# Kernel tuning notes

Hardware: AMD Instinct MI355X
Metric: run time of the kernel (lower is better)

Reference implementation:

```python
import jax, jax.numpy as jnp
import numpy as np

N = 100000   # num_nodes
E = 1600000  # num_edges
IN, HID, OUT = 128, 128, 64  # in_ft, 2*out_ft, out_ft


def setup_inputs() -> dict:
    key = jax.random.key(0)
    ks = jax.random.split(key, 8)
    x = jax.random.normal(ks[0], (N, IN), dtype=jnp.float32)
    edge_index = jax.random.randint(ks[1], (2, E), 0, N, dtype=jnp.int32)
    # Glorot-style init for GCNConv linear weights
    W1 = jax.random.normal(ks[2], (IN, HID), dtype=jnp.float32) / np.sqrt(IN).astype(np.float32)
    b1 = jnp.zeros((HID,), dtype=jnp.float32)
    W2 = jax.random.normal(ks[3], (HID, OUT), dtype=jnp.float32) / np.sqrt(HID).astype(np.float32)
    b2 = jnp.zeros((OUT,), dtype=jnp.float32)
    a = jnp.array([0.25], dtype=jnp.float32)  # shared PReLU slope (nn.PReLU default)
    return {"x": x, "edge_index": edge_index, "W1": W1, "b1": b1, "W2": W2, "b2": b2, "a": a}


def reference(x, edge_index, W1, b1, W2, b2, a):
    # PyG GCNConv semantics: add self-loops, symmetric normalization
    # norm_e = deg(src)^-1/2 * deg(dst)^-1/2, out[dst] += norm_e * (x @ W)[src] + bias
    src, dst = edge_index[0], edge_index[1]
    loops = jnp.arange(N, dtype=src.dtype)
    s = jnp.concatenate([src, loops])  # [E+N]
    d = jnp.concatenate([dst, loops])  # [E+N]
    deg = jax.ops.segment_sum(jnp.ones_like(d, dtype=x.dtype), d, num_segments=N)
    dis = jax.lax.rsqrt(deg)  # deg >= 1 thanks to self-loops
    norm = (dis[s] * dis[d])[:, None]  # [E+N, 1]

    def gcn_conv(h, W, b):
        hw = h @ W                                   # dense transform [N, F_out]
        msgs = hw[s] * norm                          # gather + scale  [E+N, F_out]
        return jax.ops.segment_sum(msgs, d, num_segments=N) + b  # scatter-add

    prelu = lambda v: jnp.where(v >= 0, v, a * v)

    h = prelu(gcn_conv(x, W1, b1))   # dropout p=0.0 -> identity
    return prelu(gcn_conv(h, W2, b2))
```

## Files before the change

kernel.cpp:

```cpp
#include <hip/hip_runtime.h>

#define N_NODES 100000
#define N_EDGES 1600000
#define BSH 9
#define NB  196
#define EPB 4096
#define CAPSH 14

typedef short bf16x8 __attribute__((ext_vector_type(8)));
typedef float f32x4 __attribute__((ext_vector_type(4)));
typedef float f32x2 __attribute__((ext_vector_type(2)));


__device__ __forceinline__ unsigned pack_bf16x2(float a, float b) {
    unsigned ua = __float_as_uint(a), ub = __float_as_uint(b);
    unsigned ra = (ua + 0x7fffu + ((ua >> 16) & 1u)) >> 16;
    unsigned rb = (ub + 0x7fffu + ((ub >> 16) & 1u)) >> 16;
    return ra | (rb << 16);
}
__device__ __forceinline__ unsigned short bf16_rne(float f) {
    unsigned u = __float_as_uint(f);
    return (unsigned short)((u + 0x7fffu + ((u >> 16) & 1u)) >> 16);
}
__device__ __forceinline__ float bf_lo(unsigned v) { return __uint_as_float(v << 16); }
__device__ __forceinline__ float bf_hi(unsigned v) { return __uint_as_float(v & 0xffff0000u); }
__device__ __forceinline__ f32x2 unpk(unsigned u) {
    f32x2 r;
    r.x = __uint_as_float(u << 16);
    r.y = __uint_as_float(u & 0xffff0000u);
    return r;
}


__global__ void cursor_init_k(int* __restrict__ cursor) {
    int b = threadIdx.x;
    if (b < NB) cursor[b] = b << CAPSH;
}

__global__ __launch_bounds__(256) void bin_k(const int* __restrict__ src,
                                             const int* __restrict__ dst,
                                             int* __restrict__ cursor,
                                             unsigned* __restrict__ binned, int E) {
    __shared__ int lhist[256];
    __shared__ int lcur[256];
    int tid = threadIdx.x;
    lhist[tid] = 0;
    __syncthreads();
    int e0 = blockIdx.x * EPB;
#pragma unroll
    for (int i = 0; i < EPB / 256; ++i) {
        int e = e0 + i * 256 + tid;
        if (e < E) atomicAdd(&lhist[dst[e] >> BSH], 1);
    }
    __syncthreads();
    {
        int c = lhist[tid];
        lcur[tid] = (tid < NB && c > 0) ? atomicAdd(&cursor[tid], c) : 0;
    }
    __syncthreads();
#pragma unroll
    for (int i = 0; i < EPB / 256; ++i) {
        int e = e0 + i * 256 + tid;
        if (e < E) {
            int d = dst[e];
            int b = d >> BSH;
            int pos = atomicAdd(&lcur[b], 1);
            if (pos < ((b + 1) << CAPSH))
                binned[pos] = ((unsigned)(d & ((1 << BSH) - 1)) << 17) | (unsigned)src[e];
        }
    }
}

__global__ void bucket_scan_k(const int* __restrict__ cursor, int* __restrict__ bucket_base) {
    __shared__ int s[256];
    int tid = threadIdx.x;
    int v = (tid < NB) ? (cursor[tid] - (tid << CAPSH)) : 0;
    s[tid] = v; __syncthreads();
    for (int off = 1; off < 256; off <<= 1) {
        int t = 0;
        if (tid >= off) t = s[tid - off];
        __syncthreads();
        s[tid] += t;
        __syncthreads();
    }
    if (tid < NB) bucket_base[tid] = s[tid] - v;
}

__global__ __launch_bounds__(256) void deg_dis_k(const unsigned* __restrict__ binned,
                                                 const int* __restrict__ cursor,
                                                 const int* __restrict__ bucket_base,
                                                 int* __restrict__ row_start,
                                                 float* __restrict__ dis, int n, int E) {
    __shared__ int lcnt[1 << BSH];
    __shared__ int ls[256];
    int b = blockIdx.x, tid = threadIdx.x;
    for (int j = tid; j < (1 << BSH); j += 256) lcnt[j] = 0;
    __syncthreads();
    int base = b << CAPSH;
    int total = cursor[b] - base;
    for (int i = tid; i < total; i += 256)
        atomicAdd(&lcnt[binned[base + i] >> 17], 1);
    __syncthreads();
    int v0 = lcnt[2 * tid], v1 = lcnt[2 * tid + 1];
    int sv = v0 + v1;
    ls[tid] = sv;
    __syncthreads();
    for (int off = 1; off < 256; off <<= 1) {
        int t = 0;
        if (tid >= off) t = ls[tid - off];
        __syncthreads();
        ls[tid] += t;
        __syncthreads();
    }
    int pre = ls[tid] - sv;
    int nbase = b << BSH;
    int bb = bucket_base[b];
    int node0 = nbase + 2 * tid, node1 = node0 + 1;
    if (node0 < n) {
        row_start[node0] = bb + pre;
        dis[node0] = rsqrtf((float)(v0 + 1));
    }
    if (node1 < n) {
        row_start[node1] = bb + pre + v0;
        dis[node1] = rsqrtf((float)(v1 + 1));
    }
    if (b == NB - 1 && tid == 255) row_start[n] = E;
}

__global__ __launch_bounds__(256) void csr_k(const unsigned* __restrict__ binned,
                                             const int* __restrict__ cursor,
                                             const int* __restrict__ row_start,
                                             const float* __restrict__ dis,
                                             uint2* __restrict__ edge, int n) {
    __shared__ int lfill[1 << BSH];
    int b = blockIdx.x, tid = threadIdx.x;
    int nbase = b << BSH;
    for (int j = tid; j < (1 << BSH); j += 256) {
        int node = nbase + j;
        lfill[j] = (node < n) ? row_start[node] : 0;
    }
    __syncthreads();
    int base = b << CAPSH;
    int total = cursor[b] - base;
    for (int i = base + tid; i < base + total; i += 256) {
        unsigned u = binned[i];
        int s = u & 0x1FFFFu;
        int dl = u >> 17;
        int pos = atomicAdd(&lfill[dl], 1);
        edge[pos] = make_uint2((unsigned)s, __float_as_uint(dis[s] * dis[nbase + dl]));
    }
}


__global__ void wt_k(const float* __restrict__ W, unsigned short* __restrict__ Wt, int C) {
    int t = blockIdx.x * 256 + threadIdx.x;
    if (t >= 128 * C) return;
    int k = t / C, c = t % C;
    int g = k >> 3, j = k & 7;
    Wt[c * 128 + ((g ^ (c & 7)) << 3) + j] = bf16_rne(W[t]);
}


template <int OUTF, bool INBF>
__global__ __launch_bounds__(256) void gemm_mfma_k(const void* __restrict__ Xv,
                                                   const unsigned short* __restrict__ Wt,
                                                   unsigned short* __restrict__ Y, int nrows) {
    constexpr int CT = OUTF / 16;
    __shared__ short lds_w[OUTF * 128];
    int tid = threadIdx.x;
    {
        const uint4* srcp = (const uint4*)Wt;
        uint4* dstp = (uint4*)lds_w;
        for (int i = tid; i < OUTF * 16; i += 256) dstp[i] = srcp[i];
    }
    __syncthreads();
    int lane = tid & 63;
    int r16 = lane & 15, kq = lane >> 4;
    int rbase = blockIdx.x * 128 + (tid >> 6) * 32;
    f32x4 acc[2][CT] = {};
#pragma unroll
    for (int kk = 0; kk < 4; ++kk) {
        int k0 = kk * 32 + kq * 8;
        bf16x8 a[2];
#pragma unroll
        for (int rt = 0; rt < 2; ++rt) {
            int row = rbase + rt * 16 + r16;
            if (row < nrows) {
                if constexpr (INBF) {
                    a[rt] = *(const bf16x8*)((const unsigned short*)Xv + (size_t)row * 128 + k0);
                } else {
                    const float* xp = (const float*)Xv + (size_t)row * 128 + k0;
                    float4 f0 = *(const float4*)xp;
                    float4 f1 = *(const float4*)(xp + 4);
                    uint4 uu = make_uint4(pack_bf16x2(f0.x, f0.y), pack_bf16x2(f0.z, f0.w),
                                          pack_bf16x2(f1.x, f1.y), pack_bf16x2(f1.z, f1.w));
                    a[rt] = *(bf16x8*)&uu;
                }
            } else {
                bf16x8 z = {0, 0, 0, 0, 0, 0, 0, 0};
                a[rt] = z;
            }
        }
#pragma unroll
        for (int c = 0; c < CT; ++c) {
            int col = c * 16 + r16;
            int gp = (kk * 4 + kq) ^ (col & 7);
            bf16x8 b = *(const bf16x8*)&lds_w[col * 128 + gp * 8];
            acc[0][c] = __builtin_amdgcn_mfma_f32_16x16x32_bf16(a[0], b, acc[0][c], 0, 0, 0);
            acc[1][c] = __builtin_amdgcn_mfma_f32_16x16x32_bf16(a[1], b, acc[1][c], 0, 0, 0);
        }
    }
#pragma unroll
    for (int rt = 0; rt < 2; ++rt) {
#pragma unroll
        for (int c = 0; c < CT; ++c) {
#pragma unroll
            for (int r = 0; r < 4; ++r) {
                int row = rbase + rt * 16 + kq * 4 + r;
                if (row < nrows)
                    Y[(size_t)row * OUTF + c * 16 + r16] = bf16_rne(acc[rt][c][r]);
            }
        }
    }
}


__global__ void agg1_k(const unsigned* __restrict__ hw, const int* __restrict__ row_start,
                       const uint2* __restrict__ edge, const float* __restrict__ dis,
                       const float* __restrict__ bias, const float* __restrict__ aslope,
                       unsigned* __restrict__ out, int n) {
    int wid = (blockIdx.x * 256 + threadIdx.x) >> 6;
    int lane = threadIdx.x & 63;
    if (wid >= n) return;
    int g = lane >> 4;
    unsigned li = lane & 15;
    unsigned rowoff = li << 4;
    const char* hwb = (const char*)hw;
    const char* edb = (const char*)edge;
    f32x2 acc[4] = {};
    int e0 = row_start[wid], e1 = row_start[wid + 1];
    for (int e = e0; e < e1; e += 16) {
        uint2 ed[4];
        uint4 v[4];
#pragma unroll
        for (int u = 0; u < 4; ++u) {
            int ee = e + u * 4 + g;
            unsigned ec = (unsigned)((ee < e1) ? ee : (e1 - 1));
            ed[u] = *(const uint2*)(edb + (ec << 3));
        }
#pragma unroll
        for (int u = 0; u < 4; ++u)
            v[u] = *(const uint4*)(hwb + ((ed[u].x << 8) | rowoff));
#pragma unroll
        for (int u = 0; u < 4; ++u) {
            float nr = (e + u * 4 + g < e1) ? __uint_as_float(ed[u].y) : 0.f;
            f32x2 nr2 = {nr, nr};
            acc[0] += unpk(v[u].x) * nr2;
            acc[1] += unpk(v[u].y) * nr2;
            acc[2] += unpk(v[u].z) * nr2;
            acc[3] += unpk(v[u].w) * nr2;
        }
    }
#pragma unroll
    for (int j = 0; j < 4; ++j) {
        acc[j].x += __shfl_xor(acc[j].x, 16, 64);
        acc[j].y += __shfl_xor(acc[j].y, 16, 64);
        acc[j].x += __shfl_xor(acc[j].x, 32, 64);
        acc[j].y += __shfl_xor(acc[j].y, 32, 64);
    }
    if (g == 0) {
        float dn = dis[wid];
        f32x2 sw2 = {dn * dn, dn * dn};
        uint4 v = *(const uint4*)(hwb + (((unsigned)wid << 8) | rowoff));
        acc[0] += unpk(v.x) * sw2;
        acc[1] += unpk(v.y) * sw2;
        acc[2] += unpk(v.z) * sw2;
        acc[3] += unpk(v.w) * sw2;
        float4 b0 = ((const float4*)bias)[li * 2];
        float4 b1 = ((const float4*)bias)[li * 2 + 1];
        float al = aslope[0];
        float r[8] = {acc[0].x + b0.x, acc[0].y + b0.y, acc[1].x + b0.z, acc[1].y + b0.w,
                      acc[2].x + b1.x, acc[2].y + b1.y, acc[3].x + b1.z, acc[3].y + b1.w};
#pragma unroll
        for (int j = 0; j < 8; ++j) r[j] = (r[j] >= 0.f) ? r[j] : al * r[j];
        uint4 o = make_uint4(pack_bf16x2(r[0], r[1]), pack_bf16x2(r[2], r[3]),
                             pack_bf16x2(r[4], r[5]), pack_bf16x2(r[6], r[7]));
        *(uint4*)(out + (size_t)wid * 64 + li * 4) = o;
    }
}

__global__ void agg2_k(const unsigned* __restrict__ hw, const int* __restrict__ row_start,
                       const uint2* __restrict__ edge, const float* __restrict__ dis,
                       const float* __restrict__ bias, const float* __restrict__ aslope,
                       float* __restrict__ out, int n) {
    int wid = (blockIdx.x * 256 + threadIdx.x) >> 6;
    int lane = threadIdx.x & 63;
    if (wid >= n) return;
    int g = lane >> 4;
    unsigned li = lane & 15;
    unsigned rowoff = li << 3;
    const char* hwb = (const char*)hw;
    const char* edb = (const char*)edge;
    f32x2 acc[2] = {};
    int e0 = row_start[wid], e1 = row_start[wid + 1];
    for (int e = e0; e < e1; e += 16) {
        uint2 ed[4];
        uint2 v[4];
#pragma unroll
        for (int u = 0; u < 4; ++u) {
            int ee = e + u * 4 + g;
            unsigned ec = (unsigned)((ee < e1) ? ee : (e1 - 1));
            ed[u] = *(const uint2*)(edb + (ec << 3));
        }
#pragma unroll
        for (int u = 0; u < 4; ++u)
            v[u] = *(const uint2*)(hwb + ((ed[u].x << 7) | rowoff));
#pragma unroll
        for (int u = 0; u < 4; ++u) {
            float nr = (e + u * 4 + g < e1) ? __uint_as_float(ed[u].y) : 0.f;
            f32x2 nr2 = {nr, nr};
            acc[0] += unpk(v[u].x) * nr2;
            acc[1] += unpk(v[u].y) * nr2;
        }
    }
#pragma unroll
    for (int j = 0; j < 2; ++j) {
        acc[j].x += __shfl_xor(acc[j].x, 16, 64);
        acc[j].y += __shfl_xor(acc[j].y, 16, 64);
        acc[j].x += __shfl_xor(acc[j].x, 32, 64);
        acc[j].y += __shfl_xor(acc[j].y, 32, 64);
    }
    if (g == 0) {
        float dn = dis[wid];
        f32x2 sw2 = {dn * dn, dn * dn};
        uint2 v = *(const uint2*)(hwb + (((unsigned)wid << 7) | rowoff));
        acc[0] += unpk(v.x) * sw2;
        acc[1] += unpk(v.y) * sw2;
        float4 b = ((const float4*)bias)[li];
        float al = aslope[0];
        float r[4] = {acc[0].x + b.x, acc[0].y + b.y, acc[1].x + b.z, acc[1].y + b.w};
#pragma unroll
        for (int j = 0; j < 4; ++j) r[j] = (r[j] >= 0.f) ? r[j] : al * r[j];
        *(float4*)(out + (size_t)wid * 64 + li * 4) = make_float4(r[0], r[1], r[2], r[3]);
    }
}


extern "C" void kernel_launch(void* const* d_in, const int* in_sizes, int n_in,
                              void* d_out, int out_size, void* d_ws, size_t ws_size,
                              hipStream_t stream) {
    const float* x  = (const float*)d_in[0];
    const int*   ei = (const int*)d_in[1];
    const int*   src = ei;
    const int*   dst = ei + N_EDGES;
    const float* W1 = (const float*)d_in[2];
    const float* b1 = (const float*)d_in[3];
    const float* W2 = (const float*)d_in[4];
    const float* b2 = (const float*)d_in[5];
    const float* a  = (const float*)d_in[6];
    float* out = (float*)d_out;

    char* ws = (char*)d_ws;
    size_t off = 0;
    auto alloc = [&](size_t bytes) -> void* {
        void* p = ws + off;
        off += (bytes + 255) & ~(size_t)255;
        return p;
    };
    int*            row_start = (int*)alloc((size_t)(N_NODES + 1) * 4);
    float*          dis       = (float*)alloc((size_t)N_NODES * 4);
    int*            cursor    = (int*)alloc(NB * 4);
    int*            bbase     = (int*)alloc(NB * 4);
    unsigned*       binned    = (unsigned*)alloc((size_t)NB * (1 << CAPSH) * 4);
    uint2*          edge      = (uint2*)alloc((size_t)N_EDGES * 8);
    unsigned*       hw1       = (unsigned*)alloc((size_t)N_NODES * 64 * 4);
    unsigned*       hbuf      = (unsigned*)alloc((size_t)N_NODES * 64 * 4);
    unsigned*       hw2       = (unsigned*)alloc((size_t)N_NODES * 32 * 4);
    unsigned short* Wt1       = (unsigned short*)alloc(128 * 128 * 2);
    unsigned short* Wt2       = (unsigned short*)alloc(64 * 128 * 2);

    int gB = (N_EDGES + EPB - 1) / EPB;

    wt_k<<<64, 256, 0, stream>>>(W1, Wt1, 128);
    wt_k<<<32, 256, 0, stream>>>(W2, Wt2, 64);

    cursor_init_k<<<1, 256, 0, stream>>>(cursor);
    bin_k<<<gB, 256, 0, stream>>>(src, dst, cursor, binned, N_EDGES);
    bucket_scan_k<<<1, 256, 0, stream>>>(cursor, bbase);
    deg_dis_k<<<NB, 256, 0, stream>>>(binned, cursor, bbase, row_start, dis, N_NODES, N_EDGES);
    csr_k<<<NB, 256, 0, stream>>>(binned, cursor, row_start, dis, edge, N_NODES);

    int gG = (N_NODES + 127) / 128;
    int gA = (N_NODES + 3) / 4;

    gemm_mfma_k<128, false><<<gG, 256, 0, stream>>>(x, Wt1, (unsigned short*)hw1, N_NODES);
    agg1_k<<<gA, 256, 0, stream>>>(hw1, row_start, edge, dis, b1, a, hbuf, N_NODES);
    gemm_mfma_k<64, true><<<gG, 256, 0, stream>>>(hbuf, Wt2, (unsigned short*)hw2, N_NODES);
    agg2_k<<<gA, 256, 0, stream>>>(hw2, row_start, edge, dis, b2, a, out, N_NODES);
}
```

Baseline: 207.6 us.

## Fuse setup kernels, co-launch binning with GEMM1, and remap aggregation to four nodes per wave

The weight-transpose and cursor-init kernels are merged into one setup launch. Edge binning and the first dense GEMM now run in a single grid, so independent memory-bound and MFMA work can overlap and one launch is removed. Both aggregation kernels now give each 16-lane group its own node instead of spreading one node across a wave, which removes the cross-group shuffle reduction. The cost is that lanes diverge across nodes with different degrees inside a wave, and the fused kernel reserves 32KB of LDS even in binning blocks, which may lower their occupancy.

```diff
diff --git a/kernel.cpp b/kernel.cpp
--- a/kernel.cpp
+++ b/kernel.cpp
@@ -6,6 +6,8 @@
 #define NB  196
 #define EPB 4096
 #define CAPSH 14
+#define GB  ((N_EDGES + EPB - 1) / EPB)
+#define GG  ((N_NODES + 127) / 128)
 
 typedef short bf16x8 __attribute__((ext_vector_type(8)));
 typedef float f32x4 __attribute__((ext_vector_type(4)));
@@ -22,8 +24,6 @@
     unsigned u = __float_as_uint(f);
     return (unsigned short)((u + 0x7fffu + ((u >> 16) & 1u)) >> 16);
 }
-__device__ __forceinline__ float bf_lo(unsigned v) { return __uint_as_float(v << 16); }
-__device__ __forceinline__ float bf_hi(unsigned v) { return __uint_as_float(v & 0xffff0000u); }
 __device__ __forceinline__ f32x2 unpk(unsigned u) {
     f32x2 r;
     r.x = __uint_as_float(u << 16);
@@ -32,41 +32,114 @@
 }
 
 
-__global__ void cursor_init_k(int* __restrict__ cursor) {
-    int b = threadIdx.x;
-    if (b < NB) cursor[b] = b << CAPSH;
-}
-
-__global__ __launch_bounds__(256) void bin_k(const int* __restrict__ src,
-                                             const int* __restrict__ dst,
-                                             int* __restrict__ cursor,
-                                             unsigned* __restrict__ binned, int E) {
+__device__ __forceinline__ void wt_body(const float* W, unsigned short* Wt, int C, int bid) {
+    int t = bid * 256 + threadIdx.x;
+    if (t >= 128 * C) return;
+    int k = t / C, c = t % C;
+    int g = k >> 3, j = k & 7;
+    Wt[c * 128 + ((g ^ (c & 7)) << 3) + j] = bf16_rne(W[t]);
+}
+
+__global__ void setup_k(const float* __restrict__ W1, unsigned short* __restrict__ Wt1,
+                        const float* __restrict__ W2, unsigned short* __restrict__ Wt2,
+                        int* __restrict__ cursor) {
+    int b = blockIdx.x;
+    if (b < 64) { wt_body(W1, Wt1, 128, b); }
+    else if (b < 96) { wt_body(W2, Wt2, 64, b - 64); }
+    else {
+        int t = threadIdx.x;
+        if (t < NB) cursor[t] = t << CAPSH;
+    }
+}
+
+
+__global__ __launch_bounds__(256) void bin_gemm1_k(
+        const int* __restrict__ src, const int* __restrict__ dst,
+        int* __restrict__ cursor, unsigned* __restrict__ binned,
+        const float* __restrict__ X, const unsigned short* __restrict__ Wt,
+        unsigned short* __restrict__ Y) {
     __shared__ int lhist[256];
     __shared__ int lcur[256];
+    __shared__ short lds_w[128 * 128];
     int tid = threadIdx.x;
-    lhist[tid] = 0;
-    __syncthreads();
-    int e0 = blockIdx.x * EPB;
-#pragma unroll
-    for (int i = 0; i < EPB / 256; ++i) {
-        int e = e0 + i * 256 + tid;
-        if (e < E) atomicAdd(&lhist[dst[e] >> BSH], 1);
-    }
-    __syncthreads();
+
+    if (blockIdx.x < GB) {
+        lhist[tid] = 0;
+        __syncthreads();
+        int e0 = blockIdx.x * EPB;
+#pragma unroll
+        for (int i = 0; i < EPB / 256; ++i) {
+            int e = e0 + i * 256 + tid;
+            if (e < N_EDGES) atomicAdd(&lhist[dst[e] >> BSH], 1);
+        }
+        __syncthreads();
+        {
+            int c = lhist[tid];
+            lcur[tid] = (tid < NB && c > 0) ? atomicAdd(&cursor[tid], c) : 0;
+        }
+        __syncthreads();
+#pragma unroll
+        for (int i = 0; i < EPB / 256; ++i) {
+            int e = e0 + i * 256 + tid;
+            if (e < N_EDGES) {
+                int d = dst[e];
+                int b = d >> BSH;
+                int pos = atomicAdd(&lcur[b], 1);
+                if (pos < ((b + 1) << CAPSH))
+                    binned[pos] = ((unsigned)(d & ((1 << BSH) - 1)) << 17) | (unsigned)src[e];
+            }
+        }
+        return;
+    }
+
     {
-        int c = lhist[tid];
-        lcur[tid] = (tid < NB && c > 0) ? atomicAdd(&cursor[tid], c) : 0;
-    }
-    __syncthreads();
-#pragma unroll
-    for (int i = 0; i < EPB / 256; ++i) {
-        int e = e0 + i * 256 + tid;
-        if (e < E) {
-            int d = dst[e];
-            int b = d >> BSH;
-            int pos = atomicAdd(&lcur[b], 1);
-            if (pos < ((b + 1) << CAPSH))
-                binned[pos] = ((unsigned)(d & ((1 << BSH) - 1)) << 17) | (unsigned)src[e];
+        const uint4* srcp = (const uint4*)Wt;
+        uint4* dstp = (uint4*)lds_w;
+        for (int i = tid; i < 128 * 16; i += 256) dstp[i] = srcp[i];
+    }
+    __syncthreads();
+    int lane = tid & 63;
+    int r16 = lane & 15, kq = lane >> 4;
+    int rbase = (blockIdx.x - GB) * 128 + (tid >> 6) * 32;
+    f32x4 acc[2][8] = {};
+#pragma unroll
+    for (int kk = 0; kk < 4; ++kk) {
+        int k0 = kk * 32 + kq * 8;
+        bf16x8 a[2];
+#pragma unroll
+        for (int rt = 0; rt < 2; ++rt) {
+            int row = rbase + rt * 16 + r16;
+            if (row < N_NODES) {
+                const float* xp = X + (size_t)row * 128 + k0;
+                float4 f0 = *(const float4*)xp;
+                float4 f1 = *(const float4*)(xp + 4);
+                uint4 uu = make_uint4(pack_bf16x2(f0.x, f0.y), pack_bf16x2(f0.z, f0.w),
+                                      pack_bf16x2(f1.x, f1.y), pack_bf16x2(f1.z, f1.w));
+                a[rt] = *(bf16x8*)&uu;
+            } else {
+                bf16x8 z = {0, 0, 0, 0, 0, 0, 0, 0};
+                a[rt] = z;
+            }
+        }
+#pragma unroll
+        for (int c = 0; c < 8; ++c) {
+            int col = c * 16 + r16;
+            int gp = (kk * 4 + kq) ^ (col & 7);
+            bf16x8 b = *(const bf16x8*)&lds_w[col * 128 + gp * 8];
+            acc[0][c] = __builtin_amdgcn_mfma_f32_16x16x32_bf16(a[0], b, acc[0][c], 0, 0, 0);
+            acc[1][c] = __builtin_amdgcn_mfma_f32_16x16x32_bf16(a[1], b, acc[1][c], 0, 0, 0);
+        }
+    }
+#pragma unroll
+    for (int rt = 0; rt < 2; ++rt) {
+#pragma unroll
+        for (int c = 0; c < 8; ++c) {
+#pragma unroll
+            for (int r = 0; r < 4; ++r) {
+                int row = rbase + rt * 16 + kq * 4 + r;
+                if (row < N_NODES)
+                    Y[(size_t)row * 128 + c * 16 + r16] = bf16_rne(acc[rt][c][r]);
+            }
         }
     }
 }
@@ -152,32 +225,21 @@
 }
 
 
-__global__ void wt_k(const float* __restrict__ W, unsigned short* __restrict__ Wt, int C) {
-    int t = blockIdx.x * 256 + threadIdx.x;
-    if (t >= 128 * C) return;
-    int k = t / C, c = t % C;
-    int g = k >> 3, j = k & 7;
-    Wt[c * 128 + ((g ^ (c & 7)) << 3) + j] = bf16_rne(W[t]);
-}
-
-
-template <int OUTF, bool INBF>
-__global__ __launch_bounds__(256) void gemm_mfma_k(const void* __restrict__ Xv,
-                                                   const unsigned short* __restrict__ Wt,
-                                                   unsigned short* __restrict__ Y, int nrows) {
-    constexpr int CT = OUTF / 16;
-    __shared__ short lds_w[OUTF * 128];
+__global__ __launch_bounds__(256) void gemm2_k(const unsigned short* __restrict__ Xv,
+                                               const unsigned short* __restrict__ Wt,
+                                               unsigned short* __restrict__ Y, int nrows) {
+    __shared__ short lds_w[64 * 128];
     int tid = threadIdx.x;
     {
         const uint4* srcp = (const uint4*)Wt;
         uint4* dstp = (uint4*)lds_w;
-        for (int i = tid; i < OUTF * 16; i += 256) dstp[i] = srcp[i];
+        for (int i = tid; i < 64 * 16; i += 256) dstp[i] = srcp[i];
     }
     __syncthreads();
     int lane = tid & 63;
     int r16 = lane & 15, kq = lane >> 4;
     int rbase = blockIdx.x * 128 + (tid >> 6) * 32;
-    f32x4 acc[2][CT] = {};
+    f32x4 acc[2][4] = {};
 #pragma unroll
     for (int kk = 0; kk < 4; ++kk) {
         int k0 = kk * 32 + kq * 8;
@@ -186,23 +248,14 @@
         for (int rt = 0; rt < 2; ++rt) {
             int row = rbase + rt * 16 + r16;
             if (row < nrows) {
-                if constexpr (INBF) {
-                    a[rt] = *(const bf16x8*)((const unsigned short*)Xv + (size_t)row * 128 + k0);
-                } else {
-                    const float* xp = (const float*)Xv + (size_t)row * 128 + k0;
-                    float4 f0 = *(const float4*)xp;
-                    float4 f1 = *(const float4*)(xp + 4);
-                    uint4 uu = make_uint4(pack_bf16x2(f0.x, f0.y), pack_bf16x2(f0.z, f0.w),
-                                          pack_bf16x2(f1.x, f1.y), pack_bf16x2(f1.z, f1.w));
-                    a[rt] = *(bf16x8*)&uu;
-                }
+                a[rt] = *(const bf16x8*)(Xv + (size_t)row * 128 + k0);
             } else {
                 bf16x8 z = {0, 0, 0, 0, 0, 0, 0, 0};
                 a[rt] = z;
             }
         }
 #pragma unroll
-        for (int c = 0; c < CT; ++c) {
+        for (int c = 0; c < 4; ++c) {
             int col = c * 16 + r16;
             int gp = (kk * 4 + kq) ^ (col & 7);
             bf16x8 b = *(const bf16x8*)&lds_w[col * 128 + gp * 8];
@@ -213,12 +266,12 @@
 #pragma unroll
     for (int rt = 0; rt < 2; ++rt) {
 #pragma unroll
-        for (int c = 0; c < CT; ++c) {
+        for (int c = 0; c < 4; ++c) {
 #pragma unroll
             for (int r = 0; r < 4; ++r) {
                 int row = rbase + rt * 16 + kq * 4 + r;
                 if (row < nrows)
-                    Y[(size_t)row * OUTF + c * 16 + r16] = bf16_rne(acc[rt][c][r]);
+                    Y[(size_t)row * 64 + c * 16 + r16] = bf16_rne(acc[rt][c][r]);
             }
         }
     }
@@ -229,49 +282,48 @@
                        const uint2* __restrict__ edge, const float* __restrict__ dis,
                        const float* __restrict__ bias, const float* __restrict__ aslope,
                        unsigned* __restrict__ out, int n) {
-    int wid = (blockIdx.x * 256 + threadIdx.x) >> 6;
+    int w = (blockIdx.x * 256 + threadIdx.x) >> 6;
     int lane = threadIdx.x & 63;
-    if (wid >= n) return;
     int g = lane >> 4;
     unsigned li = lane & 15;
+    int node = w * 4 + g;
+    bool valid = node < n;
+    int e0 = valid ? row_start[node] : 0;
+    int e1 = valid ? row_start[node + 1] : 0;
     unsigned rowoff = li << 4;
     const char* hwb = (const char*)hw;
     const char* edb = (const char*)edge;
     f32x2 acc[4] = {};
-    int e0 = row_start[wid], e1 = row_start[wid + 1];
-    for (int e = e0; e < e1; e += 16) {
-        uint2 ed[4];
-        uint4 v[4];
-#pragma unroll
-        for (int u = 0; u < 4; ++u) {
-            int ee = e + u * 4 + g;
-            unsigned ec = (unsigned)((ee < e1) ? ee : (e1 - 1));
-            ed[u] = *(const uint2*)(edb + (ec << 3));
-        }
-#pragma unroll
-        for (int u = 0; u < 4; ++u)
-            v[u] = *(const uint4*)(hwb + ((ed[u].x << 8) | rowoff));
-#pragma unroll
-        for (int u = 0; u < 4; ++u) {
-            float nr = (e + u * 4 + g < e1) ? __uint_as_float(ed[u].y) : 0.f;
-            f32x2 nr2 = {nr, nr};
-            acc[0] += unpk(v[u].x) * nr2;
-            acc[1] += unpk(v[u].y) * nr2;
-            acc[2] += unpk(v[u].z) * nr2;
-            acc[3] += unpk(v[u].w) * nr2;
-        }
-    }
-#pragma unroll
-    for (int j = 0; j < 4; ++j) {
-        acc[j].x += __shfl_xor(acc[j].x, 16, 64);
-        acc[j].y += __shfl_xor(acc[j].y, 16, 64);
-        acc[j].x += __shfl_xor(acc[j].x, 32, 64);
-        acc[j].y += __shfl_xor(acc[j].y, 32, 64);
-    }
-    if (g == 0) {
-        float dn = dis[wid];
+    int e = e0;
+    while (__any(e < e1)) {
+        if (e < e1) {
+            uint2 ed[4];
+            uint4 v[4];
+#pragma unroll
+            for (int u = 0; u < 4; ++u) {
+                int ee = e + u;
+                unsigned ec = (unsigned)((ee < e1) ? ee : (e1 - 1));
+                ed[u] = *(const uint2*)(edb + (ec << 3));
+            }
+#pragma unroll
+            for (int u = 0; u < 4; ++u)
+                v[u] = *(const uint4*)(hwb + ((ed[u].x << 8) | rowoff));
+#pragma unroll
+            for (int u = 0; u < 4; ++u) {
+                float nr = (e + u < e1) ? __uint_as_float(ed[u].y) : 0.f;
+                f32x2 nr2 = {nr, nr};
+                acc[0] += unpk(v[u].x) * nr2;
+                acc[1] += unpk(v[u].y) * nr2;
+                acc[2] += unpk(v[u].z) * nr2;
+                acc[3] += unpk(v[u].w) * nr2;
+            }
+        }
+        e += 4;
+    }
+    if (valid) {
+        float dn = dis[node];
         f32x2 sw2 = {dn * dn, dn * dn};
-        uint4 v = *(const uint4*)(hwb + (((unsigned)wid << 8) | rowoff));
+        uint4 v = *(const uint4*)(hwb + (((unsigned)node << 8) | rowoff));
         acc[0] += unpk(v.x) * sw2;
         acc[1] += unpk(v.y) * sw2;
         acc[2] += unpk(v.z) * sw2;
@@ -285,7 +337,7 @@
         for (int j = 0; j < 8; ++j) r[j] = (r[j] >= 0.f) ? r[j] : al * r[j];
         uint4 o = make_uint4(pack_bf16x2(r[0], r[1]), pack_bf16x2(r[2], r[3]),
                              pack_bf16x2(r[4], r[5]), pack_bf16x2(r[6], r[7]));
-        *(uint4*)(out + (size_t)wid * 64 + li * 4) = o;
+        *(uint4*)(out + (size_t)node * 64 + li * 4) = o;
     }
 }
 
@@ -293,47 +345,46 @@
                        const uint2* __restrict__ edge, const float* __restrict__ dis,
                        const float* __restrict__ bias, const float* __restrict__ aslope,
                        float* __restrict__ out, int n) {
-    int wid = (blockIdx.x * 256 + threadIdx.x) >> 6;
+    int w = (blockIdx.x * 256 + threadIdx.x) >> 6;
     int lane = threadIdx.x & 63;
-    if (wid >= n) return;
     int g = lane >> 4;
     unsigned li = lane & 15;
+    int node = w * 4 + g;
+    bool valid = node < n;
+    int e0 = valid ? row_start[node] : 0;
+    int e1 = valid ? row_start[node + 1] : 0;
     unsigned rowoff = li << 3;
     const char* hwb = (const char*)hw;
     const char* edb = (const char*)edge;
     f32x2 acc[2] = {};
-    int e0 = row_start[wid], e1 = row_start[wid + 1];
-    for (int e = e0; e < e1; e += 16) {
-        uint2 ed[4];
-        uint2 v[4];
-#pragma unroll
-        for (int u = 0; u < 4; ++u) {
-            int ee = e + u * 4 + g;
-            unsigned ec = (unsigned)((ee < e1) ? ee : (e1 - 1));
-            ed[u] = *(const uint2*)(edb + (ec << 3));
-        }
-#pragma unroll
-        for (int u = 0; u < 4; ++u)
-            v[u] = *(const uint2*)(hwb + ((ed[u].x << 7) | rowoff));
-#pragma unroll
-        for (int u = 0; u < 4; ++u) {
-            float nr = (e + u * 4 + g < e1) ? __uint_as_float(ed[u].y) : 0.f;
-            f32x2 nr2 = {nr, nr};
-            acc[0] += unpk(v[u].x) * nr2;
-            acc[1] += unpk(v[u].y) * nr2;
-        }
-    }
-#pragma unroll
-    for (int j = 0; j < 2; ++j) {
-        acc[j].x += __shfl_xor(acc[j].x, 16, 64);
-        acc[j].y += __shfl_xor(acc[j].y, 16, 64);
-        acc[j].x += __shfl_xor(acc[j].x, 32, 64);
-        acc[j].y += __shfl_xor(acc[j].y, 32, 64);
-    }
-    if (g == 0) {
-        float dn = dis[wid];
+    int e = e0;
+    while (__any(e < e1)) {
+        if (e < e1) {
+            uint2 ed[4];
+            uint2 v[4];
+#pragma unroll
+            for (int u = 0; u < 4; ++u) {
+                int ee = e + u;
+                unsigned ec = (unsigned)((ee < e1) ? ee : (e1 - 1));
+                ed[u] = *(const uint2*)(edb + (ec << 3));
+            }
+#pragma unroll
+            for (int u = 0; u < 4; ++u)
+                v[u] = *(const uint2*)(hwb + ((ed[u].x << 7) | rowoff));
+#pragma unroll
+            for (int u = 0; u < 4; ++u) {
+                float nr = (e + u < e1) ? __uint_as_float(ed[u].y) : 0.f;
+                f32x2 nr2 = {nr, nr};
+                acc[0] += unpk(v[u].x) * nr2;
+                acc[1] += unpk(v[u].y) * nr2;
+            }
+        }
+        e += 4;
+    }
+    if (valid) {
+        float dn = dis[node];
         f32x2 sw2 = {dn * dn, dn * dn};
-        uint2 v = *(const uint2*)(hwb + (((unsigned)wid << 7) | rowoff));
+        uint2 v = *(const uint2*)(hwb + (((unsigned)node << 7) | rowoff));
         acc[0] += unpk(v.x) * sw2;
         acc[1] += unpk(v.y) * sw2;
         float4 b = ((const float4*)bias)[li];
@@ -341,7 +392,7 @@
         float r[4] = {acc[0].x + b.x, acc[0].y + b.y, acc[1].x + b.z, acc[1].y + b.w};
 #pragma unroll
         for (int j = 0; j < 4; ++j) r[j] = (r[j] >= 0.f) ? r[j] : al * r[j];
-        *(float4*)(out + (size_t)wid * 64 + li * 4) = make_float4(r[0], r[1], r[2], r[3]);
+        *(float4*)(out + (size_t)node * 64 + li * 4) = make_float4(r[0], r[1], r[2], r[3]);
     }
 }
 
@@ -379,22 +430,18 @@
     unsigned short* Wt1       = (unsigned short*)alloc(128 * 128 * 2);
     unsigned short* Wt2       = (unsigned short*)alloc(64 * 128 * 2);
 
-    int gB = (N_EDGES + EPB - 1) / EPB;
-
-    wt_k<<<64, 256, 0, stream>>>(W1, Wt1, 128);
-    wt_k<<<32, 256, 0, stream>>>(W2, Wt2, 64);
-
-    cursor_init_k<<<1, 256, 0, stream>>>(cursor);
-    bin_k<<<gB, 256, 0, stream>>>(src, dst, cursor, binned, N_EDGES);
+    setup_k<<<97, 256, 0, stream>>>(W1, Wt1, W2, Wt2, cursor);
+    bin_gemm1_k<<<GB + GG, 256, 0, stream>>>(src, dst, cursor, binned,
+                                             x, Wt1, (unsigned short*)hw1);
     bucket_scan_k<<<1, 256, 0, stream>>>(cursor, bbase);
     deg_dis_k<<<NB, 256, 0, stream>>>(binned, cursor, bbase, row_start, dis, N_NODES, N_EDGES);
     csr_k<<<NB, 256, 0, stream>>>(binned, cursor, row_start, dis, edge, N_NODES);
 
-    int gG = (N_NODES + 127) / 128;
-    int gA = (N_NODES + 3) / 4;
-
-    gemm_mfma_k<128, false><<<gG, 256, 0, stream>>>(x, Wt1, (unsigned short*)hw1, N_NODES);
-    agg1_k<<<gA, 256, 0, stream>>>(hw1, row_start, edge, dis, b1, a, hbuf, N_NODES);
-    gemm_mfma_k<64, true><<<gG, 256, 0, stream>>>(hbuf, Wt2, (unsigned short*)hw2, N_NODES);
-    agg2_k<<<gA, 256, 0, stream>>>(hw2, row_start, edge, dis, b2, a, out, N_NODES);
-}
+    int gA = (N_NODES + 1023) / 1024;
+    gA = (N_NODES / 4 + 3) / 4;
+
+    agg1_k<<<6250, 256, 0, stream>>>(hw1, row_start, edge, dis, b1, a, hbuf, N_NODES);
+    gemm2_k<<<GG, 256, 0, stream>>>((unsigned short*)hbuf, Wt2, (unsigned short*)hw2, N_NODES);
+    agg2_k<<<6250, 256, 0, stream>>>(hw2, row_start, edge, dis, b2, a, out, N_NODES);
+    (void)gA;
+}
```

After: 186.4 us. -10.2%, faster.
